# Kernel tuning notes

Measured on AMD Instinct MI355X. Metric: run time of the kernel, lower is better.

## Reference

```python
import jax, jax.numpy as jnp
import numpy as np

B, SEQ, DIM = 2, 2048, 1024
HEADS, HEAD_DIM = 16, 64
HIDDEN = 2816
EPS = 1e-5
LN_EPS = 1e-5


def rmsnorm(x, w, eps=EPS):
    return x * jax.lax.rsqrt(jnp.mean(x * x, axis=-1, keepdims=True) + eps) * w


def layernorm(x, w, b, eps=LN_EPS):
    mu = jnp.mean(x, axis=-1, keepdims=True)
    var = jnp.mean((x - mu) ** 2, axis=-1, keepdims=True)
    return (x - mu) * jax.lax.rsqrt(var + eps) * w + b


def modulate(x, shift, scale):
    # x: [B,S,D], shift/scale: [B,D]
    return x * (1.0 + scale[:, None, :]) + shift[:, None, :]


def apply_rope(t, cos, sin):
    # t: [B,S,H,D]; cos/sin: [S, D/2] -> complex multiply on (even,odd) pairs
    t = t.reshape(*t.shape[:-1], HEAD_DIM // 2, 2)
    t0, t1 = t[..., 0], t[..., 1]
    c = cos[None, :, None, :]
    s = sin[None, :, None, :]
    o0 = t0 * c - t1 * s
    o1 = t0 * s + t1 * c
    return jnp.stack([o0, o1], axis=-1).reshape(*t.shape[:-2], HEAD_DIM)


def setup_inputs() -> dict:
    key = jax.random.key(0)
    ks = jax.random.split(key, 12)
    def w(k, shape, s=0.02):
        return jax.random.normal(k, shape, dtype=jnp.float32) * s
    x = jax.random.normal(ks[0], (B, SEQ, DIM), dtype=jnp.float32)
    adaln_input = jax.random.normal(ks[1], (B, DIM), dtype=jnp.float32)
    pos = jnp.arange(SEQ, dtype=jnp.float32)
    inv_freq = 1.0 / (10000.0 ** (jnp.arange(0, HEAD_DIM, 2, dtype=jnp.float32) / HEAD_DIM))
    ang = pos[:, None] * inv_freq[None, :]  # [S, D/2]
    return dict(
        x=x, adaln_input=adaln_input,
        freqs_cos=jnp.cos(ang), freqs_sin=jnp.sin(ang),
        wq=w(ks[2], (DIM, DIM)), wk=w(ks[3], (DIM, DIM)),
        wv=w(ks[4], (DIM, DIM)), wo=w(ks[5], (DIM, DIM)),
        q_norm_w=jnp.ones(DIM, jnp.float32), q_norm_b=jnp.zeros(DIM, jnp.float32),
        k_norm_w=jnp.ones(DIM, jnp.float32), k_norm_b=jnp.zeros(DIM, jnp.float32),
        attn_norm_w=jnp.ones(DIM, jnp.float32), ffn_norm_w=jnp.ones(DIM, jnp.float32),
        ada_w=w(ks[6], (DIM, 6 * DIM)), ada_b=jnp.zeros(6 * DIM, jnp.float32),
        w1=w(ks[7], (DIM, HIDDEN)), w2=w(ks[8], (HIDDEN, DIM)), w3=w(ks[9], (DIM, HIDDEN)),
    )


def reference(x, adaln_input, freqs_cos, freqs_sin, wq, wk, wv, wo,
              q_norm_w, q_norm_b, k_norm_w, k_norm_b,
              attn_norm_w, ffn_norm_w, ada_w, ada_b, w1, w2, w3):
    # adaLN modulation: SiLU -> Linear -> 6 chunks of [B, DIM]
    m = jax.nn.silu(adaln_input) @ ada_w + ada_b
    shift_msa, scale_msa, gate_msa, shift_mlp, scale_mlp, gate_mlp = jnp.split(m, 6, axis=1)

    # --- attention branch ---
    h = modulate(rmsnorm(x, attn_norm_w), shift_msa, scale_msa)
    xq = layernorm(h @ wq, q_norm_w, q_norm_b)
    xk = layernorm(h @ wk, k_norm_w, k_norm_b)
    xv = h @ wv
    xq = xq.reshape(B, SEQ, HEADS, HEAD_DIM)
    xk = xk.reshape(B, SEQ, HEADS, HEAD_DIM)
    xv = xv.reshape(B, SEQ, HEADS, HEAD_DIM)
    xq = apply_rope(xq, freqs_cos, freqs_sin)
    xk = apply_rope(xk, freqs_cos, freqs_sin)
    scale = 1.0 / jnp.sqrt(jnp.float32(HEAD_DIM))
    scores = jnp.einsum('bshd,bthd->bhst', xq, xk) * scale  # [B,H,S,S]
    probs = jax.nn.softmax(scores, axis=-1)
    attn = jnp.einsum('bhst,bthd->bshd', probs, xv).reshape(B, SEQ, DIM)
    attn = attn @ wo
    x = x + gate_msa[:, None, :] * attn

    # --- MLP branch (SwiGLU) ---
    h = modulate(rmsnorm(x, ffn_norm_w), shift_mlp, scale_mlp)
    ffn = (jax.nn.silu(h @ w1) * (h @ w3)) @ w2
    x = x + gate_mlp[:, None, :] * ffn
    return x
```

## Files before the change

kernel.cpp:

```cpp
#include <hip/hip_runtime.h>
#include <hip/hip_bf16.h>

#define B_   2
#define S_   2048
#define D_   1024
#define H_   16
#define HD_  64
#define HID_ 2816

typedef unsigned short u16;
typedef unsigned int   u32;
typedef __attribute__((ext_vector_type(8))) short short8;
typedef __attribute__((ext_vector_type(4))) float f32x4;
typedef __attribute__((ext_vector_type(2))) float f32x2;
typedef __attribute__((ext_vector_type(4))) u32   u32x4;
typedef __attribute__((ext_vector_type(2))) unsigned uvec2;

static __device__ __forceinline__ float bf2f(u16 u){ return __uint_as_float(((u32)u)<<16); }
static __device__ __forceinline__ u16 f2bf(float f){
  u32 u = __float_as_uint(f);
  u32 r = (u + 0x7FFFu + ((u>>16)&1u)) >> 16;
  return (u16)r;
}
static __device__ __forceinline__ u16 f2bfr(float f){
  return (u16)((__float_as_uint(f) + 0x8000u) >> 16);
}
static __device__ __forceinline__ u32 pk2(float a, float b){
  return ((__float_as_uint(a) + 0x8000u) >> 16) | ((__float_as_uint(b) + 0x8000u) & 0xFFFF0000u);
}
static __device__ __forceinline__ u32 cvtpk(float lo, float hi){
  u32 r; asm("v_cvt_pk_bf16_f32 %0, %1, %2" : "=v"(r) : "v"(lo), "v"(hi)); return r;
}
static __device__ __forceinline__ float vmax3(float a, float b, float c){
  float d; asm("v_max3_f32 %0, %1, %2, %3" : "=v"(d) : "v"(a), "v"(b), "v"(c)); return d;
}
static __device__ __forceinline__ f32x2 pkadd(f32x2 a, f32x2 b){
  f32x2 d; asm("v_pk_add_f32 %0, %1, %2" : "=v"(d) : "v"(a), "v"(b)); return d;
}
static __device__ __forceinline__ void plswap16(float x, float& a, float& b){
#if __has_builtin(__builtin_amdgcn_permlane16_swap)
  uvec2 r = __builtin_amdgcn_permlane16_swap(__float_as_uint(x), __float_as_uint(x), false, false);
  a = __uint_as_float(r[0]); b = __uint_as_float(r[1]);
#else
  a = x; b = __shfl_xor(x, 16, 64);
#endif
}
static __device__ __forceinline__ void plswap32(float x, float& a, float& b){
#if __has_builtin(__builtin_amdgcn_permlane32_swap)
  uvec2 r = __builtin_amdgcn_permlane32_swap(__float_as_uint(x), __float_as_uint(x), false, false);
  a = __uint_as_float(r[0]); b = __uint_as_float(r[1]);
#else
  a = x; b = __shfl_xor(x, 32, 64);
#endif
}

static __device__ __forceinline__ void ld4(const u16* p, float* v){
  ushort4 t = *reinterpret_cast<const ushort4*>(p);
  v[0]=bf2f(t.x); v[1]=bf2f(t.y); v[2]=bf2f(t.z); v[3]=bf2f(t.w);
}
static __device__ __forceinline__ void ld4(const float* p, float* v){
  float4 t = *reinterpret_cast<const float4*>(p);
  v[0]=t.x; v[1]=t.y; v[2]=t.z; v[3]=t.w;
}
static __device__ __forceinline__ void st4(u16* p, const float* v){
  ushort4 t; t.x=f2bf(v[0]); t.y=f2bf(v[1]); t.z=f2bf(v[2]); t.w=f2bf(v[3]);
  *reinterpret_cast<ushort4*>(p)=t;
}

static __device__ __forceinline__ float ld1g(const void* p, size_t i, bool f32){
  return f32 ? ((const float*)p)[i] : bf2f(((const u16*)p)[i]);
}
static __device__ __forceinline__ void ld4g(const void* p, size_t i, float* v, bool f32){
  if(f32){
    float4 t = *reinterpret_cast<const float4*>((const float*)p + i);
    v[0]=t.x; v[1]=t.y; v[2]=t.z; v[3]=t.w;
  }else{
    ushort4 t = *reinterpret_cast<const ushort4*>((const u16*)p + i);
    v[0]=bf2f(t.x); v[1]=bf2f(t.y); v[2]=bf2f(t.z); v[3]=bf2f(t.w);
  }
}
static __device__ __forceinline__ void st4g(void* p, size_t i, const float* v, bool f32){
  if(f32){
    float4 t; t.x=v[0]; t.y=v[1]; t.z=v[2]; t.w=v[3];
    *reinterpret_cast<float4*>((float*)p + i) = t;
  }else{
    st4((u16*)p + i, v);
  }
}

static __device__ __forceinline__ void gl2lds16(const u16* g, const u16* l){
  typedef __attribute__((address_space(3))) u16 lds_u16;
  typedef const __attribute__((address_space(1))) u16 glb_u16;
  __builtin_amdgcn_global_load_lds((glb_u16*)(uintptr_t)g,
                                   (lds_u16*)(u32)(uintptr_t)l, 16, 0, 0);
}

__global__ __launch_bounds__(256) void k_probe_zero(const u16* fc_raw, int* flag, float* m){
  int i = blockIdx.x*256 + threadIdx.x;
  if(i < 12288) m[i] = 0.f;
  if(i == 0) *flag = (fc_raw[0]==0) ? 1 : 0;
}

static __device__ __forceinline__ float blk_sum(float v, float* red){
  #pragma unroll
  for(int o=32;o;o>>=1) v += __shfl_xor(v,o,64);
  int lane = threadIdx.x & 63, w = threadIdx.x >> 6;
  if(lane==0) red[w]=v;
  __syncthreads();
  float t = red[0]+red[1]+red[2]+red[3];
  __syncthreads();
  return t;
}

__global__ __launch_bounds__(256) void k_adaln(const void* a, const void* W, const void* bias,
                                               float* m, const int* flag){
  bool f32 = flag[0] != 0;
  __shared__ float sl[2][128];
  int bk = blockIdx.y;
  {
    int bb = threadIdx.x >> 7, kk = threadIdx.x & 127;
    float x = ld1g(a, bb*D_ + bk*128 + kk, f32);
    sl[bb][kk] = x/(1.f+__expf(-x));
  }
  __syncthreads();
  int n = blockIdx.x*256 + threadIdx.x;
  float p0 = 0.f, p1 = 0.f;
  for(int kk=0;kk<128;kk++){
    float w = ld1g(W, (size_t)(bk*128+kk)*6144 + n, f32);
    p0 += sl[0][kk]*w; p1 += sl[1][kk]*w;
  }
  if(bk==0){ float bv = ld1g(bias, n, f32); p0 += bv; p1 += bv; }
  atomicAdd(&m[n], p0);
  atomicAdd(&m[6144+n], p1);
}

__global__ __launch_bounds__(256) void k_rms_mod(const void* x, const void* nw, const float* m,
                                                 u16* h, int shift_off, int scale_off,
                                                 const int* flag){
  bool f32 = flag[0] != 0;
  __shared__ float red[4];
  int row = blockIdx.x; int b = row >> 11;
  int d0 = threadIdx.x*4;
  float v[4]; ld4g(x, (size_t)row*D_ + d0, v, f32);
  float ss = v[0]*v[0]+v[1]*v[1]+v[2]*v[2]+v[3]*v[3];
  float tot = blk_sum(ss, red);
  float r = rsqrtf(tot*(1.f/D_) + 1e-5f);
  const float* mb = m + b*6144;
  float wn[4]; ld4g(nw, d0, wn, f32);
  float o[4];
  #pragma unroll
  for(int j=0;j<4;j++){
    int d = d0+j;
    o[j] = v[j]*r*wn[j]*(1.f+mb[scale_off+d]) + mb[shift_off+d];
  }
  st4(h + (size_t)row*D_ + d0, o);
}

__global__ __launch_bounds__(256) void k_resid_rms(const void* x, const u16* y, const float* m,
                                                   const void* nw, float* x2, u16* h,
                                                   const int* flag){
  bool f32 = flag[0] != 0;
  __shared__ float red[4];
  int row = blockIdx.x; int b = row >> 11;
  int d0 = threadIdx.x*4;
  size_t i4 = (size_t)row*D_ + d0;
  float xv[4], yv[4];
  ld4g(x, i4, xv, f32); ld4(y+i4, yv);
  const float* mb = m + b*6144;
  float v[4];
  #pragma unroll
  for(int j=0;j<4;j++) v[j] = xv[j] + mb[2048+d0+j]*yv[j];
  float4 t; t.x=v[0]; t.y=v[1]; t.z=v[2]; t.w=v[3];
  *reinterpret_cast<float4*>(x2+i4) = t;
  float ss = v[0]*v[0]+v[1]*v[1]+v[2]*v[2]+v[3]*v[3];
  float tot = blk_sum(ss, red);
  float r = rsqrtf(tot*(1.f/D_) + 1e-5f);
  float wn[4]; ld4g(nw, d0, wn, f32);
  float o[4];
  #pragma unroll
  for(int j=0;j<4;j++)
    o[j] = v[j]*r*wn[j]*(1.f+mb[4096+d0+j]) + mb[3072+d0+j];
  st4(h + i4, o);
}

__global__ __launch_bounds__(256) void k_ln_rope2(u16* t, const void* qw, const void* qb,
                                                  const void* kw, const void* kb2,
                                                  const void* fc, const void* fs, const int* flag){
  bool f32 = flag[0] != 0;
  __shared__ float red[4];
  int row = blockIdx.x; int s = row & (S_-1);
  const void* w  = blockIdx.y ? kw  : qw;
  const void* bb = blockIdx.y ? kb2 : qb;
  int d0 = threadIdx.x*4;
  u16* tp = t + (size_t)row*3072 + blockIdx.y*1024 + d0;
  float v[4]; ld4(tp, v);
  float sm = v[0]+v[1]+v[2]+v[3];
  float sq = v[0]*v[0]+v[1]*v[1]+v[2]*v[2]+v[3]*v[3];
  float tsm = blk_sum(sm, red);
  float tsq = blk_sum(sq, red);
  float mu  = tsm*(1.f/D_);
  float var = tsq*(1.f/D_) - mu*mu;
  float rs  = rsqrtf(var + 1e-5f);
  float wv[4], bv[4]; ld4g(w, d0, wv, f32); ld4g(bb, d0, bv, f32);
  float y[4];
  #pragma unroll
  for(int j=0;j<4;j++) y[j] = (v[j]-mu)*rs*wv[j] + bv[j];
  int pos = d0 & 63; int i0 = pos>>1;
  float c0 = ld1g(fc, s*32+i0,   f32), s0 = ld1g(fs, s*32+i0,   f32);
  float c1 = ld1g(fc, s*32+i0+1, f32), s1 = ld1g(fs, s*32+i0+1, f32);
  float o[4];
  o[0] = y[0]*c0 - y[1]*s0;
  o[1] = y[0]*s0 + y[1]*c0;
  o[2] = y[2]*c1 - y[3]*s1;
  o[3] = y[2]*s1 + y[3]*c1;
  st4(tp, o);
}

__global__ __launch_bounds__(256) void k_wt3(const void* W0, const void* W1, const void* W2,
                                             u16* WT, int Kd, int Nd, const int* flag){
  bool f32 = flag[0] != 0;
  const void* W = blockIdx.z==0 ? W0 : (blockIdx.z==1 ? W1 : W2);
  u16* dst_base = WT + (size_t)blockIdx.z * (size_t)Kd * Nd;
  __shared__ u16 L[64][72];
  int tid = threadIdx.x;
  int k0 = blockIdx.x*64, n0 = blockIdx.y*64;
  int r = tid>>2, c0 = (tid&3)*16;
  if(f32){
    const float* Wf = (const float*)W;
    #pragma unroll
    for(int j=0;j<4;j++){
      float4 t = *reinterpret_cast<const float4*>(&Wf[(size_t)(k0+r)*Nd + n0 + c0 + j*4]);
      L[r][c0+j*4+0]=f2bfr(t.x); L[r][c0+j*4+1]=f2bfr(t.y);
      L[r][c0+j*4+2]=f2bfr(t.z); L[r][c0+j*4+3]=f2bfr(t.w);
    }
  }else{
    const u16* Wh = (const u16*)W;
    *reinterpret_cast<short8*>(&L[r][c0]) =
      *reinterpret_cast<const short8*>(&Wh[(size_t)(k0+r)*Nd + n0 + c0]);
    *reinterpret_cast<short8*>(&L[r][c0+8]) =
      *reinterpret_cast<const short8*>(&Wh[(size_t)(k0+r)*Nd + n0 + c0 + 8]);
  }
  __syncthreads();
  int n = tid>>2, kk0 = (tid&3)*16;
  u16 tmp[16];
  #pragma unroll
  for(int j=0;j<16;j++) tmp[j] = L[kk0+j][n];
  u16* dst = dst_base + (size_t)(n0+n)*Kd + k0 + kk0;
  *reinterpret_cast<short8*>(dst)   = *reinterpret_cast<const short8*>(tmp);
  *reinterpret_cast<short8*>(dst+8) = *reinterpret_cast<const short8*>(tmp+8);
}

__global__ __launch_bounds__(256) void k_wt13(const void* W1, const void* W3,
                                              u16* WT, const int* flag){
  bool f32 = flag[0] != 0;
  const int Kd = 1024, Nd = HID_;
  const void* W = blockIdx.z ? W3 : W1;
  int radd = blockIdx.z ? 32 : 0;
  __shared__ u16 L[64][72];
  int tid = threadIdx.x;
  int k0 = blockIdx.x*64, n0 = blockIdx.y*64;
  int r = tid>>2, c0 = (tid&3)*16;
  if(f32){
    const float* Wf = (const float*)W;
    #pragma unroll
    for(int j=0;j<4;j++){
      float4 t = *reinterpret_cast<const float4*>(&Wf[(size_t)(k0+r)*Nd + n0 + c0 + j*4]);
      L[r][c0+j*4+0]=f2bfr(t.x); L[r][c0+j*4+1]=f2bfr(t.y);
      L[r][c0+j*4+2]=f2bfr(t.z); L[r][c0+j*4+3]=f2bfr(t.w);
    }
  }else{
    const u16* Wh = (const u16*)W;
    *reinterpret_cast<short8*>(&L[r][c0]) =
      *reinterpret_cast<const short8*>(&Wh[(size_t)(k0+r)*Nd + n0 + c0]);
    *reinterpret_cast<short8*>(&L[r][c0+8]) =
      *reinterpret_cast<const short8*>(&Wh[(size_t)(k0+r)*Nd + n0 + c0 + 8]);
  }
  __syncthreads();
  int n = tid>>2, kk0 = (tid&3)*16;
  u16 tmp[16];
  #pragma unroll
  for(int j=0;j<16;j++) tmp[j] = L[kk0+j][n];
  int nglob = n0 + n;
  int rw = ((nglob>>5)<<6) + (nglob&31) + radd;
  u16* dst = WT + (size_t)rw*Kd + k0 + kk0;
  *reinterpret_cast<short8*>(dst)   = *reinterpret_cast<const short8*>(tmp);
  *reinterpret_cast<short8*>(dst+8) = *reinterpret_cast<const short8*>(tmp+8);
}

template<int TM, int EPI>
__global__ __launch_bounds__(256) void k_gemm_mfma(const u16* A, int lda, const u16* BT, int ldb,
                                                   u16* C, int N, int K,
                                                   const float* x2, const float* mg,
                                                   void* outp, const int* flag){
  __shared__ __align__(16) u16 As[TM*64];
  __shared__ __align__(16) u16 Bs[128*64];
  int tid = threadIdx.x, lane = tid&63, w = tid>>6;
  int col = lane&15, quad = lane>>4;
  int row0 = blockIdx.y*TM, col0 = blockIdx.x*128;
  const u16* Ab = A  + (size_t)row0*lda;
  const u16* Bb = BT + (size_t)col0*ldb;
  constexpr int MI = TM/32;
  int wm = (w>>1)*(TM/2);
  int wn = (w&1)*64;
  f32x4 acc[MI][4];
  #pragma unroll
  for(int i=0;i<MI;i++)
    #pragma unroll
    for(int j=0;j<4;j++) acc[i][j] = (f32x4){0.f,0.f,0.f,0.f};

  for(int k0=0;k0<K;k0+=64){
    __syncthreads();
    #pragma unroll
    for(int i=0;i<TM/32;i++){
      int c = i*256 + w*64 + lane;
      int r = c>>3, s = c&7, gs = s ^ (r&7);
      gl2lds16(Ab + (size_t)r*lda + k0 + gs*8, As + (size_t)c*8);
    }
    #pragma unroll
    for(int i=0;i<4;i++){
      int c = i*256 + w*64 + lane;
      int r = c>>3, s = c&7, gs = s ^ (r&7);
      gl2lds16(Bb + (size_t)r*ldb + k0 + gs*8, Bs + (size_t)c*8);
    }
    __syncthreads();
    #pragma unroll
    for(int ks=0;ks<64;ks+=32){
      short8 af[MI], bfr[4];
      #pragma unroll
      for(int mi=0;mi<MI;mi++){
        int r = wm+mi*16+col;
        int sch = ((ks>>3) + quad) ^ (col&7);
        af[mi] = *reinterpret_cast<const short8*>(&As[r*64 + sch*8]);
      }
      #pragma unroll
      for(int ni=0;ni<4;ni++){
        int r = wn+ni*16+col;
        int sch = ((ks>>3) + quad) ^ (col&7);
        bfr[ni] = *reinterpret_cast<const short8*>(&Bs[r*64 + sch*8]);
      }
      #pragma unroll
      for(int mi=0;mi<MI;mi++)
        #pragma unroll
        for(int ni=0;ni<4;ni++)
          acc[mi][ni] = __builtin_amdgcn_mfma_f32_16x16x32_bf16(af[mi], bfr[ni], acc[mi][ni], 0,0,0);
    }
  }
  if constexpr(EPI==0){
    #pragma unroll
    for(int mi=0;mi<MI;mi++)
      #pragma unroll
      for(int r=0;r<4;r++){
        size_t rowoff = (size_t)(row0+wm+mi*16+quad*4+r)*N + col0 + wn;
        #pragma unroll
        for(int ni=0;ni<4;ni++)
          C[rowoff + ni*16 + col] = f2bfr(acc[mi][ni][r]);
      }
  } else if constexpr(EPI==1){
    int cb = blockIdx.x*64 + (wn?32:0) + col;
    #pragma unroll
    for(int mi=0;mi<MI;mi++)
      #pragma unroll
      for(int r=0;r<4;r++){
        int row = row0+wm+mi*16+quad*4+r;
        u16* gp = C + (size_t)row*HID_ + cb;
        #pragma unroll
        for(int ni=0;ni<2;ni++){
          float a = acc[mi][ni][r], cc = acc[mi][ni+2][r];
          float sv = a * __builtin_amdgcn_rcpf(1.f + __builtin_amdgcn_exp2f(-1.4426950f*a));
          gp[ni*16] = f2bfr(sv*cc);
        }
      }
  } else {
    bool f32o = flag[0] != 0;
    #pragma unroll
    for(int mi=0;mi<MI;mi++)
      #pragma unroll
      for(int r=0;r<4;r++){
        int row = row0+wm+mi*16+quad*4+r;
        int b = row >> 11;
        #pragma unroll
        for(int ni=0;ni<4;ni++){
          int cc = col0 + wn + ni*16 + col;
          float v = x2[(size_t)row*D_ + cc] + mg[b*6144 + 5120 + cc]*acc[mi][ni][r];
          if(f32o) ((float*)outp)[(size_t)row*D_ + cc] = v;
          else     ((u16*)outp)[(size_t)row*D_ + cc]   = f2bfr(v);
        }
      }
  }
}

__global__ __launch_bounds__(256) void k_vt(const u16* v, int vstr, u16* vt){
  __shared__ u16 L[64][72];
  int tid = threadIdx.x;
  int wg = blockIdx.x;
  int kblk = wg & 31; int bh = wg >> 5; int h = bh & 15, b = bh >> 4;
  int row = tid>>2, c0 = (tid&3)*16;
  const u16* src = v + (size_t)(b*S_ + kblk*64 + row)*vstr + h*HD_ + c0;
  *reinterpret_cast<short8*>(&L[row][c0])   = *reinterpret_cast<const short8*>(src);
  *reinterpret_cast<short8*>(&L[row][c0+8]) = *reinterpret_cast<const short8*>(src+8);
  __syncthreads();
  int hd = tid>>2, k0 = (tid&3)*16;
  u16 tmp[16];
  #pragma unroll
  for(int j=0;j<16;j++) tmp[j] = L[k0+j][hd];
  u16* dst = vt + ((size_t)bh*HD_ + hd)*S_ + kblk*64 + k0;
  *reinterpret_cast<short8*>(dst)   = *reinterpret_cast<const short8*>(tmp);
  *reinterpret_cast<short8*>(dst+8) = *reinterpret_cast<const short8*>(tmp+8);
}

__global__ __launch_bounds__(256) void k_attn_mfma(const u16* q, const u16* k, const u16* vt,
                                                   u16* o, int qks){
  __shared__ __align__(16) u16 Ks[2][64*64];
  __shared__ __align__(16) u16 Vs[2][64*64];
  int tid = threadIdx.x, lane = tid & 63, wid = tid >> 6;
  int col = lane & 15, quad = lane >> 4;
  int c7 = col & 7;
  int wg = ((blockIdx.x & 7) << 7) + (blockIdx.x >> 3);
  int qblk = wg & 31; int bh = wg >> 5; int h = bh & 15, b = bh >> 4;

  const u16* kb  = k  + (size_t)b*S_*qks + h*HD_;
  const u16* vtb = vt + (size_t)bh*HD_*S_;

  short8 qa0, qa1;
  {
    const float qscale = 0.18033688f;
    const u16* qp = q + (size_t)(b*S_ + qblk*64 + wid*16 + col)*qks + h*HD_ + quad*8;
    short8 t0 = *reinterpret_cast<const short8*>(qp);
    short8 t1 = *reinterpret_cast<const short8*>(qp + 32);
    #pragma unroll
    for(int j=0;j<8;j++){
      qa0[j] = (short)f2bf(bf2f((u16)t0[j])*qscale);
      qa1[j] = (short)f2bf(bf2f((u16)t1[j])*qscale);
    }
  }
  short8 vone;
  #pragma unroll
  for(int j=0;j<8;j++) vone[j] = (short)0x3F80;

  float m_i = -1e30f;
  f32x2 nm = (f32x2){1e30f, 1e30f};
  f32x4 accl = (f32x4){0.f,0.f,0.f,0.f};
  f32x4 acc[4];
  #pragma unroll
  for(int t=0;t<4;t++) acc[t] = (f32x4){0.f,0.f,0.f,0.f};

  int l0 = tid>>3;
  int l1 = 32 + l0;
  int gs = ((tid&7) ^ (l0&7))*8;
  int kl0 = 32*(l0>>5) + 8*((l0>>2)&3) + 4*((l0>>4)&1) + (l0&3);
  int kl1 = 32*(l1>>5) + 8*((l1>>2)&3) + 4*((l1>>4)&1) + (l1&3);
  const u16* kp0 = kb + (size_t)kl0*qks + gs;
  const u16* kp1 = kb + (size_t)kl1*qks + gs;
  const u16* vp0 = vtb + (size_t)l0*S_ + gs;
  const u16* vp1 = vtb + (size_t)l1*S_ + gs;

  gl2lds16(kp0, &Ks[0][tid*8]);
  gl2lds16(kp1, &Ks[0][2048 + tid*8]);
  gl2lds16(vp0, &Vs[0][tid*8]);
  gl2lds16(vp1, &Vs[0][2048 + tid*8]);

  for(int i=0;i<32;i++){
    __syncthreads();
    const u16* Kc = Ks[i&1];
    const u16* Vc = Vs[i&1];
    if(i < 31){
      size_t off = (size_t)(i+1)*64;
      u16* Kn = (u16*)Ks[(i+1)&1];
      u16* Vn = (u16*)Vs[(i+1)&1];
      gl2lds16(kp0 + off*qks, &Kn[tid*8]);
      gl2lds16(kp1 + off*qks, &Kn[2048 + tid*8]);
      gl2lds16(vp0 + off,     &Vn[tid*8]);
      gl2lds16(vp1 + off,     &Vn[2048 + tid*8]);
    }

    f32x4 st[4];
    #pragma unroll
    for(int mt=0;mt<4;mt++){
      st[mt] = (f32x4){0.f,0.f,0.f,0.f};
      short8 ka0 = *reinterpret_cast<const short8*>(&Kc[(mt*16+col)*64 + ((quad  ) ^ c7)*8]);
      short8 ka1 = *reinterpret_cast<const short8*>(&Kc[(mt*16+col)*64 + ((quad+4) ^ c7)*8]);
      st[mt] = __builtin_amdgcn_mfma_f32_16x16x32_bf16(ka0, qa0, st[mt], 0,0,0);
      st[mt] = __builtin_amdgcn_mfma_f32_16x16x32_bf16(ka1, qa1, st[mt], 0,0,0);
    }
    float t0 = vmax3(st[0][0], st[0][1], st[0][2]);
    float t1 = vmax3(st[0][3], st[1][0], st[1][1]);
    float t2 = vmax3(st[1][2], st[1][3], st[2][0]);
    float t3 = vmax3(st[2][1], st[2][2], st[2][3]);
    float t4 = vmax3(st[3][0], st[3][1], st[3][2]);
    float cm = fmaxf(vmax3(t0, t1, t2), vmax3(t3, t4, st[3][3]));
    { float a, bb2; plswap16(cm, a, bb2); cm = fmaxf(a, bb2);
      plswap32(cm, a, bb2); cm = fmaxf(a, bb2); }
    if(__any(cm - m_i > 8.f)){
      float mn = fmaxf(m_i, cm);
      float al = __builtin_amdgcn_exp2f(m_i - mn);
      m_i = mn;
      nm = (f32x2){-mn, -mn};
      accl[0] *= al;
      #pragma unroll
      for(int t=0;t<4;t++) acc[t] *= al;
    }
    float pe[4][4];
    #pragma unroll
    for(int mt=0;mt<4;mt++){
      f32x2 lo = pkadd(st[mt].xy, nm);
      f32x2 hi = pkadd(st[mt].zw, nm);
      pe[mt][0] = __builtin_amdgcn_exp2f(lo.x);
      pe[mt][1] = __builtin_amdgcn_exp2f(lo.y);
      pe[mt][2] = __builtin_amdgcn_exp2f(hi.x);
      pe[mt][3] = __builtin_amdgcn_exp2f(hi.y);
    }
    #pragma unroll
    for(int w=0;w<2;w++){
      u32x4 pw;
      pw[0] = cvtpk(pe[2*w][0],   pe[2*w][1]);
      pw[1] = cvtpk(pe[2*w][2],   pe[2*w][3]);
      pw[2] = cvtpk(pe[2*w+1][0], pe[2*w+1][1]);
      pw[3] = cvtpk(pe[2*w+1][2], pe[2*w+1][3]);
      short8 pb = *reinterpret_cast<short8*>(&pw);
      #pragma unroll
      for(int ht=0;ht<4;ht++){
        short8 vf = *reinterpret_cast<const short8*>(&Vc[(ht*16+col)*64 + ((w*4+quad) ^ c7)*8]);
        acc[ht] = __builtin_amdgcn_mfma_f32_16x16x32_bf16(vf, pb, acc[ht], 0,0,0);
      }
      accl = __builtin_amdgcn_mfma_f32_16x16x32_bf16(vone, pb, accl, 0,0,0);
    }
  }
  float inv = __builtin_amdgcn_rcpf(accl[0]);
  u16* ob = o + (size_t)(b*S_ + qblk*64 + wid*16 + col)*D_ + h*HD_;
  #pragma unroll
  for(int ht=0;ht<4;ht++){
    uint2 t;
    t.x = cvtpk(acc[ht][0]*inv, acc[ht][1]*inv);
    t.y = cvtpk(acc[ht][2]*inv, acc[ht][3]*inv);
    *reinterpret_cast<uint2*>(ob + ht*16 + quad*4) = t;
  }
}

extern "C" void kernel_launch(void* const* d_in, const int* in_sizes, int n_in,
                              void* d_out, int out_size, void* d_ws, size_t ws_size,
                              hipStream_t stream){
  const void* x   = d_in[0];
  const void* ada = d_in[1];
  const void* fc  = d_in[2];
  const void* fs  = d_in[3];
  const void* wq  = d_in[4];
  const void* wk  = d_in[5];
  const void* wv  = d_in[6];
  const void* wo  = d_in[7];
  const void* qnw = d_in[8];
  const void* qnb = d_in[9];
  const void* knw = d_in[10];
  const void* knb = d_in[11];
  const void* anw = d_in[12];
  const void* fnw = d_in[13];
  const void* aw  = d_in[14];
  const void* ab  = d_in[15];
  const void* w1  = d_in[16];
  const void* w2  = d_in[17];
  const void* w3  = d_in[18];
  char* ws = (char*)d_ws;
  const size_t MB = 1u<<20;

  int*   flag = (int*)ws;
  float* m    = (float*)(ws + 4096);
  u16*  hbuf  = (u16*)(ws + 1*MB);
  u16*  xqkv  = (u16*)(ws + 9*MB);
  float* x2   = (float*)(ws + 9*MB);
  u16*  proj  = (u16*)(ws + 25*MB);
  u16*  wreg  = (u16*)(ws + 33*MB);
  u16*  g     = (u16*)(ws + 45*MB);
  u16*  vt    = wreg;

  dim3 blk(256);

  k_probe_zero<<<dim3(48), blk, 0, stream>>>((const u16*)fc, flag, m);
  k_adaln<<<dim3(24,8), blk, 0, stream>>>(ada, aw, ab, m, flag);
  k_rms_mod<<<dim3(B_*S_), blk, 0, stream>>>(x, anw, m, hbuf, 0, 1024, flag);

  k_wt3<<<dim3(16,16,3), blk, 0, stream>>>(wq, wk, wv, wreg, 1024, 1024, flag);
  k_gemm_mfma<128,0><<<dim3(24,32), blk, 0, stream>>>(hbuf, 1024, wreg, 1024, xqkv,
                                                      3072, 1024, nullptr, nullptr, nullptr, flag);

  k_ln_rope2<<<dim3(B_*S_,2), blk, 0, stream>>>(xqkv, qnw, qnb, knw, knb, fc, fs, flag);
  k_vt<<<dim3(B_*H_*S_/64), blk, 0, stream>>>(xqkv + 2048, 3072, vt);
  k_attn_mfma<<<dim3(B_*H_*S_/64), blk, 0, stream>>>(xqkv, xqkv + 1024, vt, hbuf, 3072);

  k_wt3<<<dim3(16,16,1), blk, 0, stream>>>(wo, wo, wo, wreg, 1024, 1024, flag);
  k_gemm_mfma<64,0><<<dim3(8,64), blk, 0, stream>>>(hbuf, 1024, wreg, 1024, proj,
                                                    1024, 1024, nullptr, nullptr, nullptr, flag);
  k_resid_rms<<<dim3(B_*S_), blk, 0, stream>>>(x, proj, m, fnw, x2, hbuf, flag);

  k_wt13<<<dim3(16,44,2), blk, 0, stream>>>(w1, w3, wreg, flag);
  k_gemm_mfma<128,1><<<dim3(44,32), blk, 0, stream>>>(hbuf, 1024, wreg, 1024, g,
                                                      5632, 1024, nullptr, nullptr, nullptr, flag);
  k_wt3<<<dim3(44,16,1), blk, 0, stream>>>(w2, w2, w2, wreg, 2816, 1024, flag);
  k_gemm_mfma<64,2><<<dim3(8,64), blk, 0, stream>>>(g, 2816, wreg, 2816, nullptr,
                                                    1024, 2816, x2, m, d_out, flag);
}
```

Before: 439.0 us.

## Process two query tiles per attention workgroup to reuse K/V LDS tiles

The attention kernel now handles 128 query rows per workgroup, as two 64-row groups that share each K and V tile staged in LDS. This halves global K/V traffic and LDS fills per query row, and gives each wave independent MFMA chains to interleave. MFMA sections are wrapped in s_setprio raises, and launch bounds request two workgroups per SIMD. The cost is double the accumulator and score registers per thread plus half as many workgroups (512), which could lower occupancy or cause spills.

```diff
diff --git a/kernel.cpp b/kernel.cpp
--- a/kernel.cpp
+++ b/kernel.cpp
@@ -408,41 +408,47 @@
   *reinterpret_cast<short8*>(dst+8) = *reinterpret_cast<const short8*>(tmp+8);
 }
 
-__global__ __launch_bounds__(256) void k_attn_mfma(const u16* q, const u16* k, const u16* vt,
-                                                   u16* o, int qks){
+__global__ __launch_bounds__(256, 2) void k_attn_mfma(const u16* q, const u16* k, const u16* vt,
+                                                      u16* o, int qks){
   __shared__ __align__(16) u16 Ks[2][64*64];
   __shared__ __align__(16) u16 Vs[2][64*64];
   int tid = threadIdx.x, lane = tid & 63, wid = tid >> 6;
   int col = lane & 15, quad = lane >> 4;
   int c7 = col & 7;
-  int wg = ((blockIdx.x & 7) << 7) + (blockIdx.x >> 3);
-  int qblk = wg & 31; int bh = wg >> 5; int h = bh & 15, b = bh >> 4;
+  int wg = ((blockIdx.x & 7) << 6) + (blockIdx.x >> 3);
+  int qb = wg & 15; int bh = wg >> 4; int h = bh & 15, b = bh >> 4;
 
   const u16* kb  = k  + (size_t)b*S_*qks + h*HD_;
   const u16* vtb = vt + (size_t)bh*HD_*S_;
 
-  short8 qa0, qa1;
+  short8 qa[2][2];
   {
     const float qscale = 0.18033688f;
-    const u16* qp = q + (size_t)(b*S_ + qblk*64 + wid*16 + col)*qks + h*HD_ + quad*8;
-    short8 t0 = *reinterpret_cast<const short8*>(qp);
-    short8 t1 = *reinterpret_cast<const short8*>(qp + 32);
-    #pragma unroll
-    for(int j=0;j<8;j++){
-      qa0[j] = (short)f2bf(bf2f((u16)t0[j])*qscale);
-      qa1[j] = (short)f2bf(bf2f((u16)t1[j])*qscale);
+    const u16* qp = q + (size_t)(b*S_ + qb*128 + wid*16 + col)*qks + h*HD_ + quad*8;
+    #pragma unroll
+    for(int g=0;g<2;g++){
+      short8 t0 = *reinterpret_cast<const short8*>(qp + (size_t)g*64*qks);
+      short8 t1 = *reinterpret_cast<const short8*>(qp + (size_t)g*64*qks + 32);
+      #pragma unroll
+      for(int j=0;j<8;j++){
+        qa[g][0][j] = (short)f2bf(bf2f((u16)t0[j])*qscale);
+        qa[g][1][j] = (short)f2bf(bf2f((u16)t1[j])*qscale);
+      }
     }
   }
   short8 vone;
   #pragma unroll
   for(int j=0;j<8;j++) vone[j] = (short)0x3F80;
 
-  float m_i = -1e30f;
-  f32x2 nm = (f32x2){1e30f, 1e30f};
-  f32x4 accl = (f32x4){0.f,0.f,0.f,0.f};
-  f32x4 acc[4];
-  #pragma unroll
-  for(int t=0;t<4;t++) acc[t] = (f32x4){0.f,0.f,0.f,0.f};
+  float m_i[2] = {-1e30f, -1e30f};
+  f32x2 nm[2]; nm[0] = (f32x2){1e30f,1e30f}; nm[1] = (f32x2){1e30f,1e30f};
+  f32x4 accl[2];
+  accl[0] = (f32x4){0.f,0.f,0.f,0.f}; accl[1] = (f32x4){0.f,0.f,0.f,0.f};
+  f32x4 acc[2][4];
+  #pragma unroll
+  for(int g=0;g<2;g++)
+    #pragma unroll
+    for(int t=0;t<4;t++) acc[g][t] = (f32x4){0.f,0.f,0.f,0.f};
 
   int l0 = tid>>3;
   int l1 = 32 + l0;
@@ -473,66 +479,86 @@
       gl2lds16(vp1 + off,     &Vn[2048 + tid*8]);
     }
 
-    f32x4 st[4];
+    f32x4 st[2][4];
+    __builtin_amdgcn_s_setprio(1);
     #pragma unroll
     for(int mt=0;mt<4;mt++){
-      st[mt] = (f32x4){0.f,0.f,0.f,0.f};
       short8 ka0 = *reinterpret_cast<const short8*>(&Kc[(mt*16+col)*64 + ((quad  ) ^ c7)*8]);
       short8 ka1 = *reinterpret_cast<const short8*>(&Kc[(mt*16+col)*64 + ((quad+4) ^ c7)*8]);
-      st[mt] = __builtin_amdgcn_mfma_f32_16x16x32_bf16(ka0, qa0, st[mt], 0,0,0);
-      st[mt] = __builtin_amdgcn_mfma_f32_16x16x32_bf16(ka1, qa1, st[mt], 0,0,0);
-    }
-    float t0 = vmax3(st[0][0], st[0][1], st[0][2]);
-    float t1 = vmax3(st[0][3], st[1][0], st[1][1]);
-    float t2 = vmax3(st[1][2], st[1][3], st[2][0]);
-    float t3 = vmax3(st[2][1], st[2][2], st[2][3]);
-    float t4 = vmax3(st[3][0], st[3][1], st[3][2]);
-    float cm = fmaxf(vmax3(t0, t1, t2), vmax3(t3, t4, st[3][3]));
-    { float a, bb2; plswap16(cm, a, bb2); cm = fmaxf(a, bb2);
-      plswap32(cm, a, bb2); cm = fmaxf(a, bb2); }
-    if(__any(cm - m_i > 8.f)){
-      float mn = fmaxf(m_i, cm);
-      float al = __builtin_amdgcn_exp2f(m_i - mn);
-      m_i = mn;
-      nm = (f32x2){-mn, -mn};
-      accl[0] *= al;
-      #pragma unroll
-      for(int t=0;t<4;t++) acc[t] *= al;
-    }
-    float pe[4][4];
-    #pragma unroll
-    for(int mt=0;mt<4;mt++){
-      f32x2 lo = pkadd(st[mt].xy, nm);
-      f32x2 hi = pkadd(st[mt].zw, nm);
-      pe[mt][0] = __builtin_amdgcn_exp2f(lo.x);
-      pe[mt][1] = __builtin_amdgcn_exp2f(lo.y);
-      pe[mt][2] = __builtin_amdgcn_exp2f(hi.x);
-      pe[mt][3] = __builtin_amdgcn_exp2f(hi.y);
-    }
+      f32x4 z = (f32x4){0.f,0.f,0.f,0.f};
+      st[0][mt] = __builtin_amdgcn_mfma_f32_16x16x32_bf16(ka0, qa[0][0], z, 0,0,0);
+      st[1][mt] = __builtin_amdgcn_mfma_f32_16x16x32_bf16(ka0, qa[1][0], z, 0,0,0);
+      st[0][mt] = __builtin_amdgcn_mfma_f32_16x16x32_bf16(ka1, qa[0][1], st[0][mt], 0,0,0);
+      st[1][mt] = __builtin_amdgcn_mfma_f32_16x16x32_bf16(ka1, qa[1][1], st[1][mt], 0,0,0);
+    }
+    __builtin_amdgcn_s_setprio(0);
+
+    u32x4 pws[2][2];
+    #pragma unroll
+    for(int g=0;g<2;g++){
+      float t0 = vmax3(st[g][0][0], st[g][0][1], st[g][0][2]);
+      float t1 = vmax3(st[g][0][3], st[g][1][0], st[g][1][1]);
+      float t2 = vmax3(st[g][1][2], st[g][1][3], st[g][2][0]);
+      float t3 = vmax3(st[g][2][1], st[g][2][2], st[g][2][3]);
+      float t4 = vmax3(st[g][3][0], st[g][3][1], st[g][3][2]);
+      float cm = fmaxf(vmax3(t0, t1, t2), vmax3(t3, t4, st[g][3][3]));
+      { float a, bb2; plswap16(cm, a, bb2); cm = fmaxf(a, bb2);
+        plswap32(cm, a, bb2); cm = fmaxf(a, bb2); }
+      if(__any(cm - m_i[g] > 8.f)){
+        float mn = fmaxf(m_i[g], cm);
+        float al = __builtin_amdgcn_exp2f(m_i[g] - mn);
+        m_i[g] = mn;
+        nm[g] = (f32x2){-mn, -mn};
+        accl[g][0] *= al;
+        #pragma unroll
+        for(int t=0;t<4;t++) acc[g][t] *= al;
+      }
+      float pe[4][4];
+      #pragma unroll
+      for(int mt=0;mt<4;mt++){
+        f32x2 lo = pkadd(st[g][mt].xy, nm[g]);
+        f32x2 hi = pkadd(st[g][mt].zw, nm[g]);
+        pe[mt][0] = __builtin_amdgcn_exp2f(lo.x);
+        pe[mt][1] = __builtin_amdgcn_exp2f(lo.y);
+        pe[mt][2] = __builtin_amdgcn_exp2f(hi.x);
+        pe[mt][3] = __builtin_amdgcn_exp2f(hi.y);
+      }
+      #pragma unroll
+      for(int w=0;w<2;w++){
+        pws[g][w][0] = cvtpk(pe[2*w][0],   pe[2*w][1]);
+        pws[g][w][1] = cvtpk(pe[2*w][2],   pe[2*w][3]);
+        pws[g][w][2] = cvtpk(pe[2*w+1][0], pe[2*w+1][1]);
+        pws[g][w][3] = cvtpk(pe[2*w+1][2], pe[2*w+1][3]);
+      }
+    }
+
+    __builtin_amdgcn_s_setprio(1);
     #pragma unroll
     for(int w=0;w<2;w++){
-      u32x4 pw;
-      pw[0] = cvtpk(pe[2*w][0],   pe[2*w][1]);
-      pw[1] = cvtpk(pe[2*w][2],   pe[2*w][3]);
-      pw[2] = cvtpk(pe[2*w+1][0], pe[2*w+1][1]);
-      pw[3] = cvtpk(pe[2*w+1][2], pe[2*w+1][3]);
-      short8 pb = *reinterpret_cast<short8*>(&pw);
+      short8 pb0 = *reinterpret_cast<short8*>(&pws[0][w]);
+      short8 pb1 = *reinterpret_cast<short8*>(&pws[1][w]);
       #pragma unroll
       for(int ht=0;ht<4;ht++){
         short8 vf = *reinterpret_cast<const short8*>(&Vc[(ht*16+col)*64 + ((w*4+quad) ^ c7)*8]);
-        acc[ht] = __builtin_amdgcn_mfma_f32_16x16x32_bf16(vf, pb, acc[ht], 0,0,0);
-      }
-      accl = __builtin_amdgcn_mfma_f32_16x16x32_bf16(vone, pb, accl, 0,0,0);
-    }
-  }
-  float inv = __builtin_amdgcn_rcpf(accl[0]);
-  u16* ob = o + (size_t)(b*S_ + qblk*64 + wid*16 + col)*D_ + h*HD_;
-  #pragma unroll
-  for(int ht=0;ht<4;ht++){
-    uint2 t;
-    t.x = cvtpk(acc[ht][0]*inv, acc[ht][1]*inv);
-    t.y = cvtpk(acc[ht][2]*inv, acc[ht][3]*inv);
-    *reinterpret_cast<uint2*>(ob + ht*16 + quad*4) = t;
+        acc[0][ht] = __builtin_amdgcn_mfma_f32_16x16x32_bf16(vf, pb0, acc[0][ht], 0,0,0);
+        acc[1][ht] = __builtin_amdgcn_mfma_f32_16x16x32_bf16(vf, pb1, acc[1][ht], 0,0,0);
+      }
+      accl[0] = __builtin_amdgcn_mfma_f32_16x16x32_bf16(vone, pb0, accl[0], 0,0,0);
+      accl[1] = __builtin_amdgcn_mfma_f32_16x16x32_bf16(vone, pb1, accl[1], 0,0,0);
+    }
+    __builtin_amdgcn_s_setprio(0);
+  }
+  #pragma unroll
+  for(int g=0;g<2;g++){
+    float inv = __builtin_amdgcn_rcpf(accl[g][0]);
+    u16* ob = o + (size_t)(b*S_ + qb*128 + g*64 + wid*16 + col)*D_ + h*HD_;
+    #pragma unroll
+    for(int ht=0;ht<4;ht++){
+      uint2 t;
+      t.x = cvtpk(acc[g][ht][0]*inv, acc[g][ht][1]*inv);
+      t.y = cvtpk(acc[g][ht][2]*inv, acc[g][ht][3]*inv);
+      *reinterpret_cast<uint2*>(ob + ht*16 + quad*4) = t;
+    }
   }
 }
 
@@ -583,7 +609,7 @@
 
   k_ln_rope2<<<dim3(B_*S_,2), blk, 0, stream>>>(xqkv, qnw, qnb, knw, knb, fc, fs, flag);
   k_vt<<<dim3(B_*H_*S_/64), blk, 0, stream>>>(xqkv + 2048, 3072, vt);
-  k_attn_mfma<<<dim3(B_*H_*S_/64), blk, 0, stream>>>(xqkv, xqkv + 1024, vt, hbuf, 3072);
+  k_attn_mfma<<<dim3(B_*H_*S_/128), blk, 0, stream>>>(xqkv, xqkv + 1024, vt, hbuf, 3072);
 
   k_wt3<<<dim3(16,16,1), blk, 0, stream>>>(wo, wo, wo, wreg, 1024, 1024, flag);
   k_gemm_mfma<64,0><<<dim3(8,64), blk, 0, stream>>>(hbuf, 1024, wreg, 1024, proj,
```

Measured after the change: 418.9 us. 4.6% less time.
